# Kernel tuning notes

Measured on AMD Instinct MI355X. Metric: run time of the kernel, lower is better.

The kernel has to match this reference:

```python
import jax, jax.numpy as jnp
import numpy as np

N = 100000      # num_nodes
E = 1_600_000   # edges (avg degree 16)
D_IN = 128
D_H = 128
D_OUT = 128


def setup_inputs() -> dict:
    key = jax.random.key(0)
    ks = jax.random.split(key, 11)
    x = jax.random.normal(ks[0], (N, D_IN), dtype=jnp.float32)
    edge_index = jax.random.randint(ks[1], (2, E), 0, N, dtype=jnp.int32)
    s_in = 1.0 / np.sqrt(D_IN)
    s_h = 1.0 / np.sqrt(D_H)
    return {
        "x": x,
        "edge_index": edge_index,
        "W_neigh1": jax.random.uniform(ks[2], (D_H, D_IN), jnp.float32, -s_in, s_in),
        "b_neigh1": jax.random.uniform(ks[3], (D_H,), jnp.float32, -s_in, s_in),
        "W_self1": jax.random.uniform(ks[4], (D_H, D_IN), jnp.float32, -s_in, s_in),
        "b_self1": jax.random.uniform(ks[5], (D_H,), jnp.float32, -s_in, s_in),
        "W_neigh2": jax.random.uniform(ks[6], (D_OUT, D_H), jnp.float32, -s_h, s_h),
        "b_neigh2": jax.random.uniform(ks[7], (D_OUT,), jnp.float32, -s_h, s_h),
        "W_self2": jax.random.uniform(ks[8], (D_OUT, D_H), jnp.float32, -s_h, s_h),
        "b_self2": jax.random.uniform(ks[9], (D_OUT,), jnp.float32, -s_h, s_h),
    }


def reference(x, edge_index, W_neigh1, b_neigh1, W_self1, b_self1,
              W_neigh2, b_neigh2, W_self2, b_self2):
    src, dst = edge_index[0], edge_index[1]
    n = x.shape[0]
    # row-normalized adjacency: deg over dst (row index), clamped to >= 1
    deg = jax.ops.segment_sum(jnp.ones(src.shape[0], x.dtype), dst, num_segments=n)
    inv_deg = 1.0 / jnp.maximum(deg, 1.0)  # [N]

    def agg(h):  # mean aggregation: (A_rownorm @ h)
        return jax.ops.segment_sum(h[src], dst, num_segments=n) * inv_deg[:, None]

    h1 = agg(x) @ W_neigh1.T + b_neigh1 + x @ W_self1.T + b_self1
    h1 = jax.nn.relu(h1)
    # dropout omitted (eval-mode / deterministic reference)
    h2 = agg(h1) @ W_neigh2.T + b_neigh2 + h1 @ W_self2.T + b_self2
    return h2
```

## Files before the change

kernel.cpp:

```cpp
#include <hip/hip_runtime.h>
#include <hip/hip_bf16.h>


typedef __attribute__((ext_vector_type(8))) short short8;
typedef __attribute__((ext_vector_type(4))) float float4_;

#define NBMAX 512

__device__ __forceinline__ unsigned short f2bf(float f) {
    unsigned int u = __float_as_uint(f);
    unsigned int r = (u + 0x7FFFu + ((u >> 16) & 1u)) >> 16;
    return (unsigned short)r;
}

__global__ __launch_bounds__(256) void bucket_count(const int* __restrict__ dst, int E, int NB,
                                                    int* __restrict__ hist) {
    __shared__ int h[NBMAX];
    int tid = threadIdx.x;
    for (int b = tid; b < NB; b += 256) h[b] = 0;
    __syncthreads();
    int base = blockIdx.x * 4096;
    for (int i = 0; i < 16; i++) {
        int e = base + i * 256 + tid;
        if (e < E) atomicAdd(&h[dst[e] >> 8], 1);
    }
    __syncthreads();
    int* out = hist + (size_t)blockIdx.x * NB;
    for (int b = tid; b < NB; b += 256) out[b] = h[b];
}

__global__ __launch_bounds__(256) void blk_scan(const int* __restrict__ hist, int nblk, int NB,
                                                int* __restrict__ baseT,
                                                int* __restrict__ bucketCnt) {
    __shared__ int sd[256];
    __shared__ int carryS;
    int b = blockIdx.x, tid = threadIdx.x;
    if (tid == 0) carryS = 0;
    __syncthreads();
    for (int c0 = 0; c0 < nblk; c0 += 256) {
        int i = c0 + tid;
        int v = (i < nblk) ? hist[(size_t)i * NB + b] : 0;
        sd[tid] = v;
        __syncthreads();
        for (int off = 1; off < 256; off <<= 1) {
            int x = sd[tid];
            int y = (tid >= off) ? sd[tid - off] : 0;
            __syncthreads();
            sd[tid] = x + y;
            __syncthreads();
        }
        int carry = carryS;
        if (i < nblk) baseT[(size_t)i * NB + b] = carry + sd[tid] - v;
        __syncthreads();
        if (tid == 255) carryS = carry + sd[255];
        __syncthreads();
    }
    if (tid == 0) bucketCnt[b] = carryS;
}

__device__ __forceinline__ void scan_buckets(const int* __restrict__ bucketCnt, int NB,
                                             int* bOffs, int* sc) {
    int tid = threadIdx.x;
    int b0 = 2 * tid, b1 = 2 * tid + 1;
    int c0 = (b0 < NB) ? bucketCnt[b0] : 0;
    int c1 = (b1 < NB) ? bucketCnt[b1] : 0;
    int ts = c0 + c1;
    sc[tid] = ts;
    __syncthreads();
    for (int off = 1; off < 256; off <<= 1) {
        int x = sc[tid];
        int y = (tid >= off) ? sc[tid - off] : 0;
        __syncthreads();
        sc[tid] = x + y;
        __syncthreads();
    }
    int excl = sc[tid] - ts;
    bOffs[b0] = excl;
    bOffs[b1] = excl + c0;
    __syncthreads();
}

__global__ __launch_bounds__(256) void partition_wprep(
    const int* __restrict__ src, const int* __restrict__ dst, int E, int NB, int partBlocks,
    const int* __restrict__ bucketCnt, const int* __restrict__ baseT,
    unsigned int* __restrict__ bucketBuf,
    const float* __restrict__ Wn1, const float* __restrict__ Ws1,
    const float* __restrict__ bn1, const float* __restrict__ bs1,
    const float* __restrict__ Wn2, const float* __restrict__ Ws2,
    const float* __restrict__ bn2, const float* __restrict__ bs2,
    unsigned short* __restrict__ Bpre, float* __restrict__ biasPre) {
    int tid = threadIdx.x;
    if ((int)blockIdx.x >= partBlocks) {
        int wb = blockIdx.x - partBlocks;
        int l = wb >> 4;
        const float* Wn = l ? Wn2 : Wn1;
        const float* Ws = l ? Ws2 : Ws1;
        int fi = (wb & 15) * 256 + tid;
        int kt = fi >> 9;
        int nt = (fi >> 6) & 7;
        int lane = fi & 63;
        int o = nt * 16 + (lane & 15);
        int k = kt * 32 + (lane >> 4) * 8;
        const float* srcp = (k < 128) ? (Wn + o * 128 + k) : (Ws + o * 128 + (k - 128));
        short8 v;
#pragma unroll
        for (int j = 0; j < 8; j++) v[j] = (short)f2bf(srcp[j]);
        ((short8*)(Bpre + (size_t)l * 32768))[fi] = v;
        if ((wb & 15) == 0 && tid < 128) {
            const float* bn = l ? bn2 : bn1;
            const float* bs = l ? bs2 : bs1;
            biasPre[l * 128 + tid] = bn[tid] + bs[tid];
        }
        return;
    }
    __shared__ int cnt[NBMAX];
    __shared__ int bOffs[NBMAX];
    __shared__ int gb[NBMAX];
    __shared__ int sc[256];
    scan_buckets(bucketCnt, NB, bOffs, sc);
    for (int b = tid; b < NB; b += 256) {
        cnt[b] = 0;
        gb[b] = bOffs[b] + baseT[(size_t)blockIdx.x * NB + b];
    }
    __syncthreads();
    int eb = blockIdx.x * 4096;
    unsigned int pk[16];
    int bk[16], rk[16];
    for (int i = 0; i < 16; i++) {
        int e = eb + i * 256 + tid;
        if (e < E) {
            int d = dst[e];
            bk[i] = d >> 8;
            pk[i] = (unsigned)src[e] | ((unsigned)(d & 255) << 24);
            rk[i] = atomicAdd(&cnt[bk[i]], 1);
        } else {
            bk[i] = -1;
        }
    }
    __syncthreads();
    for (int i = 0; i < 16; i++)
        if (bk[i] >= 0) bucketBuf[gb[bk[i]] + rk[i]] = pk[i];
}

__global__ __launch_bounds__(256) void csrbuild_cvt(
    const unsigned int* __restrict__ bucketBuf, const int* __restrict__ bucketCnt,
    int N, int NB, int* __restrict__ deg, int* __restrict__ offs, int* __restrict__ sortedSrc,
    const float* __restrict__ xin, unsigned int* __restrict__ xb, int n2) {
    int tid = threadIdx.x;
    if ((int)blockIdx.x >= NB) {
        int cb = blockIdx.x - NB;
        int base = cb * 2048 + tid;
        if (xb) {
#pragma unroll
            for (int i = 0; i < 8; i++) {
                int t = base + i * 256;
                if (t < n2) {
                    float2 v = ((const float2*)xin)[t];
                    xb[t] = (unsigned)f2bf(v.x) | ((unsigned)f2bf(v.y) << 16);
                }
            }
        }
        return;
    }
    __shared__ int bOffs[NBMAX];
    __shared__ int h[256];
    __shared__ int sc[256];
    __shared__ int cur[256];
    scan_buckets(bucketCnt, NB, bOffs, sc);
    int b = blockIdx.x;
    int n0 = b << 8;
    int bo = bOffs[b];
    int cnt = bucketCnt[b];
    h[tid] = 0;
    __syncthreads();
    for (int i = tid; i < cnt; i += 256) atomicAdd(&h[bucketBuf[bo + i] >> 24], 1);
    __syncthreads();
    int v = h[tid];
    sc[tid] = v;
    __syncthreads();
    for (int off = 1; off < 256; off <<= 1) {
        int x = sc[tid];
        int y = (tid >= off) ? sc[tid - off] : 0;
        __syncthreads();
        sc[tid] = x + y;
        __syncthreads();
    }
    int excl = sc[tid] - v;
    cur[tid] = bo + excl;
    int n = n0 + tid;
    if (n < N) {
        deg[n] = v;
        offs[n] = bo + excl;
    }
    __syncthreads();
    for (int i = tid; i < cnt; i += 256) {
        unsigned int pv = bucketBuf[bo + i];
        int pos = atomicAdd(&cur[pv >> 24], 1);
        sortedSrc[pos] = (int)(pv & 0xFFFFFFu);
    }
}

__global__ __launch_bounds__(256) void agg_bf16_kernel(
    const unsigned int* __restrict__ srcFeats,
    const int* __restrict__ deg, const int* __restrict__ offs,
    const int* __restrict__ sortedSrc,
    unsigned int* __restrict__ dst, int Nn) {
    int wave = threadIdx.x >> 6, lane = threadIdx.x & 63;
    int n = blockIdx.x * 4 + wave;
    if (n >= Nn) return;
    int d = deg[n], st = offs[n];
    float a0 = 0.f, a1 = 0.f;
    int j = 0;
    for (; j + 16 <= d; j += 16) {
        unsigned int uu[16];
#pragma unroll
        for (int u = 0; u < 16; u++) {
            int s = __builtin_amdgcn_readfirstlane(sortedSrc[st + j + u]);
            uu[u] = (srcFeats + (size_t)s * 64)[lane];
        }
#pragma unroll
        for (int u = 0; u < 16; u++) {
            a0 += __uint_as_float(uu[u] << 16);
            a1 += __uint_as_float(uu[u] & 0xFFFF0000u);
        }
    }
    for (; j + 8 <= d; j += 8) {
        unsigned int uu[8];
#pragma unroll
        for (int u = 0; u < 8; u++) {
            int s = __builtin_amdgcn_readfirstlane(sortedSrc[st + j + u]);
            uu[u] = (srcFeats + (size_t)s * 64)[lane];
        }
#pragma unroll
        for (int u = 0; u < 8; u++) {
            a0 += __uint_as_float(uu[u] << 16);
            a1 += __uint_as_float(uu[u] & 0xFFFF0000u);
        }
    }
    for (; j < d; j++) {
        int s = __builtin_amdgcn_readfirstlane(sortedSrc[st + j]);
        unsigned int u = (srcFeats + (size_t)s * 64)[lane];
        a0 += __uint_as_float(u << 16);
        a1 += __uint_as_float(u & 0xFFFF0000u);
    }
    float inv = 1.0f / (float)max(d, 1);
    dst[(size_t)n * 64 + lane] = (unsigned)f2bf(a0 * inv) | ((unsigned)f2bf(a1 * inv) << 16);
}

__global__ __launch_bounds__(256) void agg_f32_kernel(
    const float* __restrict__ srcFeats,
    const int* __restrict__ deg, const int* __restrict__ offs,
    const int* __restrict__ sortedSrc,
    unsigned int* __restrict__ dst, int Nn) {
    int wave = threadIdx.x >> 6, lane = threadIdx.x & 63;
    int n = blockIdx.x * 4 + wave;
    if (n >= Nn) return;
    int d = deg[n], st = offs[n];
    float a0 = 0.f, a1 = 0.f;
    int j = 0;
    for (; j + 8 <= d; j += 8) {
        float2 v[8];
#pragma unroll
        for (int u = 0; u < 8; u++) {
            int s = __builtin_amdgcn_readfirstlane(sortedSrc[st + j + u]);
            v[u] = ((const float2*)(srcFeats + (size_t)s * 128))[lane];
        }
#pragma unroll
        for (int u = 0; u < 8; u++) {
            a0 += v[u].x;
            a1 += v[u].y;
        }
    }
    for (; j < d; j++) {
        int s = __builtin_amdgcn_readfirstlane(sortedSrc[st + j]);
        float2 v = ((const float2*)(srcFeats + (size_t)s * 128))[lane];
        a0 += v.x;
        a1 += v.y;
    }
    float inv = 1.0f / (float)max(d, 1);
    dst[(size_t)n * 64 + lane] = (unsigned)f2bf(a0 * inv) | ((unsigned)f2bf(a1 * inv) << 16);
}

__global__ __launch_bounds__(256) void gemm_kernel(
    const unsigned short* __restrict__ Aagg, const void* Aself,
    const unsigned short* __restrict__ Bpre, const float* __restrict__ biasPre,
    void* Out, int relu, int selfF32, int outBf16, int Nrows) {
    __shared__ unsigned short ldsB[8 * 8 * 64 * 8];
    __shared__ float biasS[128];
    int tid = threadIdx.x;

#pragma unroll
    for (int i = 0; i < 16; i++) {
        int fi = tid + 256 * i;
        ((short8*)ldsB)[fi] = ((const short8*)Bpre)[fi];
    }
    if (tid < 128) biasS[tid] = biasPre[tid];
    __syncthreads();

    int wave = tid >> 6, lane = tid & 63;
    int quad = lane >> 4, mr = lane & 15;
    int rowBase = blockIdx.x * 128 + wave * 32;

    short8 af[2][8];
#pragma unroll
    for (int mt = 0; mt < 2; mt++) {
        int row = rowBase + mt * 16 + mr;
        if (row >= Nrows) row = Nrows - 1;
        const unsigned short* pa = Aagg + (size_t)row * 128 + quad * 8;
#pragma unroll
        for (int kt = 0; kt < 4; kt++) af[mt][kt] = *(const short8*)(pa + kt * 32);
        if (selfF32) {
            const float* ps = (const float*)Aself + (size_t)row * 128 + quad * 8;
#pragma unroll
            for (int kt = 0; kt < 4; kt++) {
                float4_ f0 = *(const float4_*)(ps + kt * 32);
                float4_ f1 = *(const float4_*)(ps + kt * 32 + 4);
                short8 t;
#pragma unroll
                for (int j = 0; j < 4; j++) {
                    t[j] = (short)f2bf(f0[j]);
                    t[4 + j] = (short)f2bf(f1[j]);
                }
                af[mt][4 + kt] = t;
            }
        } else {
            const unsigned short* ps = (const unsigned short*)Aself + (size_t)row * 128 + quad * 8;
#pragma unroll
            for (int kt = 0; kt < 4; kt++) af[mt][4 + kt] = *(const short8*)(ps + kt * 32);
        }
    }

    float4_ acc[2][8];
    float4_ z = {0.f, 0.f, 0.f, 0.f};
#pragma unroll
    for (int mt = 0; mt < 2; mt++)
#pragma unroll
        for (int nt = 0; nt < 8; nt++) acc[mt][nt] = z;

#pragma unroll
    for (int kt = 0; kt < 8; kt++) {
#pragma unroll
        for (int nt = 0; nt < 8; nt++) {
            short8 b = *(const short8*)(ldsB + ((size_t)(kt * 8 + nt) * 64 + lane) * 8);
            acc[0][nt] = __builtin_amdgcn_mfma_f32_16x16x32_bf16(af[0][kt], b, acc[0][nt], 0, 0, 0);
            acc[1][nt] = __builtin_amdgcn_mfma_f32_16x16x32_bf16(af[1][kt], b, acc[1][nt], 0, 0, 0);
        }
    }

    for (int mt = 0; mt < 2; mt++) {
        for (int nt = 0; nt < 8; nt++) {
            int col = nt * 16 + mr;
            float bv = biasS[col];
            for (int r = 0; r < 4; r++) {
                int row = rowBase + mt * 16 + quad * 4 + r;
                if (row < Nrows) {
                    float v = acc[mt][nt][r] + bv;
                    if (relu) v = fmaxf(v, 0.f);
                    if (outBf16)
                        ((unsigned short*)Out)[(size_t)row * 128 + col] = f2bf(v);
                    else
                        ((float*)Out)[(size_t)row * 128 + col] = v;
                }
            }
        }
    }
}

extern "C" void kernel_launch(void* const* d_in, const int* in_sizes, int n_in,
                              void* d_out, int out_size, void* d_ws, size_t ws_size,
                              hipStream_t stream) {
    const float* x = (const float*)d_in[0];
    const int* ei = (const int*)d_in[1];
    const float* Wn1 = (const float*)d_in[2];
    const float* bn1 = (const float*)d_in[3];
    const float* Ws1 = (const float*)d_in[4];
    const float* bs1 = (const float*)d_in[5];
    const float* Wn2 = (const float*)d_in[6];
    const float* bn2 = (const float*)d_in[7];
    const float* Ws2 = (const float*)d_in[8];
    const float* bs2 = (const float*)d_in[9];

    const int N = in_sizes[0] / 128;
    const int E = in_sizes[1] / 2;
    const int* srcI = ei;
    const int* dstI = ei + E;
    const int NB = (N + 255) >> 8;
    const int ebBlocks = (E + 4095) / 4096;

    char* ws = (char*)d_ws;
    size_t off = 0;
    auto alloc = [&](size_t bytes) -> void* {
        void* p = ws + off;
        off += (bytes + 255) & ~(size_t)255;
        return p;
    };
    int* deg = (int*)alloc((size_t)N * 4);
    int* offs = (int*)alloc((size_t)N * 4);
    int* bucketCnt = (int*)alloc((NBMAX + 1) * 4);
    int* hist = (int*)alloc((size_t)ebBlocks * NB * 4);
    int* baseT = (int*)alloc((size_t)ebBlocks * NB * 4);
    unsigned short* Bpre = (unsigned short*)alloc(2 * 32768 * 2);
    float* biasPre = (float*)alloc(2 * 128 * 4);
    int* sortedSrc = (int*)alloc((size_t)E * 4);
    unsigned short* Aagg = (unsigned short*)alloc((size_t)N * 128 * 2);
    size_t baseNeed = off;
    size_t bf16Buf = ((size_t)N * 128 * 2 + 255) & ~(size_t)255;
    bool bigWs = (ws_size >= baseNeed + 2 * bf16Buf);
    unsigned int* xb = nullptr;
    unsigned short* h1b = nullptr;
    if (bigWs) {
        xb = (unsigned int*)alloc((size_t)N * 128 * 2);
        h1b = (unsigned short*)alloc((size_t)N * 128 * 2);
    }
    unsigned int* bucketBuf = (unsigned int*)Aagg;

    int n2 = N * 64;
    int cvtBlocks = bigWs ? (n2 + 2047) / 2048 : 0;
    bucket_count<<<ebBlocks, 256, 0, stream>>>(dstI, E, NB, hist);
    blk_scan<<<NB, 256, 0, stream>>>(hist, ebBlocks, NB, baseT, bucketCnt);
    partition_wprep<<<ebBlocks + 32, 256, 0, stream>>>(
        srcI, dstI, E, NB, ebBlocks, bucketCnt, baseT, bucketBuf,
        Wn1, Ws1, bn1, bs1, Wn2, Ws2, bn2, bs2, Bpre, biasPre);
    csrbuild_cvt<<<NB + cvtBlocks, 256, 0, stream>>>(bucketBuf, bucketCnt, N, NB, deg, offs,
                                                     sortedSrc, x, xb, n2);

    int aggBlocks = (N + 3) / 4;
    int gemmBlocks = (N + 127) / 128;

    if (bigWs) {
        agg_bf16_kernel<<<aggBlocks, 256, 0, stream>>>(xb, deg, offs, sortedSrc,
                                                       (unsigned int*)Aagg, N);
        gemm_kernel<<<gemmBlocks, 256, 0, stream>>>(Aagg, xb, Bpre, biasPre, h1b, 1, 0, 1, N);
        agg_bf16_kernel<<<aggBlocks, 256, 0, stream>>>((const unsigned int*)h1b, deg, offs,
                                                       sortedSrc, (unsigned int*)Aagg, N);
        gemm_kernel<<<gemmBlocks, 256, 0, stream>>>(Aagg, h1b, Bpre + 32768, biasPre + 128,
                                                    d_out, 0, 0, 0, N);
    } else {
        float* h1 = (float*)d_out;
        agg_f32_kernel<<<aggBlocks, 256, 0, stream>>>(x, deg, offs, sortedSrc,
                                                      (unsigned int*)Aagg, N);
        gemm_kernel<<<gemmBlocks, 256, 0, stream>>>(Aagg, x, Bpre, biasPre, h1, 1, 1, 0, N);
        agg_f32_kernel<<<aggBlocks, 256, 0, stream>>>(h1, deg, offs, sortedSrc,
                                                      (unsigned int*)Aagg, N);
        gemm_kernel<<<gemmBlocks, 256, 0, stream>>>(Aagg, h1, Bpre + 32768, biasPre + 128,
                                                    d_out, 0, 1, 0, N);
    }
}
```

Before: 348.2 us.

## Drop LDS staging of weights in GEMM and stream A fragments per k-step

The GEMM kernel no longer copies the 64KB pre-packed weight matrix and bias into shared memory. It now reads B fragments directly from global memory, where they are expected to hit in cache. A fragments are loaded per k-step instead of all preloaded into registers, and launch bounds request 4 blocks per CU. This removes the LDS footprint and the barrier, which limited occupancy, and cuts register pressure. The cost is repeated global/L2 traffic for the weights in every block and less latency hiding for the A loads.

```diff
diff --git a/kernel.cpp b/kernel.cpp
--- a/kernel.cpp
+++ b/kernel.cpp
@@ -281,76 +281,59 @@
     dst[(size_t)n * 64 + lane] = (unsigned)f2bf(a0 * inv) | ((unsigned)f2bf(a1 * inv) << 16);
 }
 
-__global__ __launch_bounds__(256) void gemm_kernel(
+__global__ __launch_bounds__(256, 4) void gemm_kernel(
     const unsigned short* __restrict__ Aagg, const void* Aself,
     const unsigned short* __restrict__ Bpre, const float* __restrict__ biasPre,
     void* Out, int relu, int selfF32, int outBf16, int Nrows) {
-    __shared__ unsigned short ldsB[8 * 8 * 64 * 8];
-    __shared__ float biasS[128];
     int tid = threadIdx.x;
-
-#pragma unroll
-    for (int i = 0; i < 16; i++) {
-        int fi = tid + 256 * i;
-        ((short8*)ldsB)[fi] = ((const short8*)Bpre)[fi];
-    }
-    if (tid < 128) biasS[tid] = biasPre[tid];
-    __syncthreads();
-
     int wave = tid >> 6, lane = tid & 63;
     int quad = lane >> 4, mr = lane & 15;
     int rowBase = blockIdx.x * 128 + wave * 32;
 
-    short8 af[2][8];
-#pragma unroll
-    for (int mt = 0; mt < 2; mt++) {
-        int row = rowBase + mt * 16 + mr;
-        if (row >= Nrows) row = Nrows - 1;
-        const unsigned short* pa = Aagg + (size_t)row * 128 + quad * 8;
-#pragma unroll
-        for (int kt = 0; kt < 4; kt++) af[mt][kt] = *(const short8*)(pa + kt * 32);
-        if (selfF32) {
-            const float* ps = (const float*)Aself + (size_t)row * 128 + quad * 8;
-#pragma unroll
-            for (int kt = 0; kt < 4; kt++) {
-                float4_ f0 = *(const float4_*)(ps + kt * 32);
-                float4_ f1 = *(const float4_*)(ps + kt * 32 + 4);
+    float4_ acc[2][8];
+    float4_ z = {0.f, 0.f, 0.f, 0.f};
+#pragma unroll
+    for (int mt = 0; mt < 2; mt++)
+#pragma unroll
+        for (int nt = 0; nt < 8; nt++) acc[mt][nt] = z;
+
+#pragma unroll
+    for (int kt = 0; kt < 8; kt++) {
+        int kk = (kt & 3) * 32 + quad * 8;
+        short8 a[2];
+#pragma unroll
+        for (int mt = 0; mt < 2; mt++) {
+            int row = rowBase + mt * 16 + mr;
+            if (row >= Nrows) row = Nrows - 1;
+            if (kt < 4) {
+                a[mt] = *(const short8*)(Aagg + (size_t)row * 128 + kk);
+            } else if (selfF32) {
+                const float* p = (const float*)Aself + (size_t)row * 128 + kk;
+                float4_ f0 = *(const float4_*)p;
+                float4_ f1 = *(const float4_*)(p + 4);
                 short8 t;
 #pragma unroll
                 for (int j = 0; j < 4; j++) {
                     t[j] = (short)f2bf(f0[j]);
                     t[4 + j] = (short)f2bf(f1[j]);
                 }
-                af[mt][4 + kt] = t;
+                a[mt] = t;
+            } else {
+                a[mt] = *(const short8*)((const unsigned short*)Aself + (size_t)row * 128 + kk);
             }
-        } else {
-            const unsigned short* ps = (const unsigned short*)Aself + (size_t)row * 128 + quad * 8;
-#pragma unroll
-            for (int kt = 0; kt < 4; kt++) af[mt][4 + kt] = *(const short8*)(ps + kt * 32);
-        }
-    }
-
-    float4_ acc[2][8];
-    float4_ z = {0.f, 0.f, 0.f, 0.f};
-#pragma unroll
-    for (int mt = 0; mt < 2; mt++)
-#pragma unroll
-        for (int nt = 0; nt < 8; nt++) acc[mt][nt] = z;
-
-#pragma unroll
-    for (int kt = 0; kt < 8; kt++) {
+        }
 #pragma unroll
         for (int nt = 0; nt < 8; nt++) {
-            short8 b = *(const short8*)(ldsB + ((size_t)(kt * 8 + nt) * 64 + lane) * 8);
-            acc[0][nt] = __builtin_amdgcn_mfma_f32_16x16x32_bf16(af[0][kt], b, acc[0][nt], 0, 0, 0);
-            acc[1][nt] = __builtin_amdgcn_mfma_f32_16x16x32_bf16(af[1][kt], b, acc[1][nt], 0, 0, 0);
+            short8 b = *(const short8*)(Bpre + ((size_t)(kt * 8 + nt) * 64 + lane) * 8);
+            acc[0][nt] = __builtin_amdgcn_mfma_f32_16x16x32_bf16(a[0], b, acc[0][nt], 0, 0, 0);
+            acc[1][nt] = __builtin_amdgcn_mfma_f32_16x16x32_bf16(a[1], b, acc[1][nt], 0, 0, 0);
         }
     }
 
     for (int mt = 0; mt < 2; mt++) {
         for (int nt = 0; nt < 8; nt++) {
             int col = nt * 16 + mr;
-            float bv = biasS[col];
+            float bv = biasPre[col];
             for (int r = 0; r < 4; r++) {
                 int row = rowBase + mt * 16 + quad * 4 + r;
                 if (row < Nrows) {
```

Measured after the change: 353.3 us. No clear change (+1.5%).
